# Performance work log

Measured on AMD Instinct MI355X. Metric: run time of the kernel, lower is better.

## Reference

```python
import jax, jax.numpy as jnp
import numpy as np

GROUP = 128  # per-group quantization along the input dimension


def _quantize_int4(w):
    """Asymmetric INT4 per-group quantization. w: [out, in] -> (q, scale, zero).
    q: int32 in [0,15], shape [out, in//GROUP, GROUP]; scale/zero: [out, in//GROUP]."""
    o, i = w.shape
    wg = w.reshape(o, i // GROUP, GROUP)
    mn = wg.min(axis=-1)
    mx = wg.max(axis=-1)
    scale = (mx - mn) / 15.0
    scale = jnp.where(scale == 0, jnp.float32(1.0), scale)
    zero = jnp.clip(jnp.round(-mn / scale), 0.0, 15.0)
    q = jnp.clip(jnp.round(wg / scale[..., None]) + zero[..., None], 0.0, 15.0).astype(jnp.int32)
    return q, scale.astype(jnp.float32), zero.astype(jnp.float32)


def _dequant(q, s, z):
    """(q - zero) * scale, regrouped back to [out, in]."""
    w = (q.astype(jnp.float32) - z[..., None]) * s[..., None]
    return w.reshape(q.shape[0], -1)


def setup_inputs() -> dict:
    key = jax.random.key(0)
    ks = jax.random.split(key, 5)
    B, D_IN, D_H, D_OUT = 512, 2048, 8192, 2048
    x = jax.random.normal(ks[0], (B, D_IN), dtype=jnp.float32)
    w1 = jax.random.normal(ks[1], (D_H, D_IN), dtype=jnp.float32) * 0.02
    b1 = jax.random.normal(ks[2], (D_H,), dtype=jnp.float32) * 0.01
    w2 = jax.random.normal(ks[3], (D_OUT, D_H), dtype=jnp.float32) * 0.02
    b2 = jax.random.normal(ks[4], (D_OUT,), dtype=jnp.float32) * 0.01
    q1, s1, z1 = _quantize_int4(w1)
    q2, s2, z2 = _quantize_int4(w2)
    return {"x": x, "q1": q1, "s1": s1, "z1": z1, "b1": b1,
            "q2": q2, "s2": s2, "z2": z2, "b2": b2}


def reference(x, q1, s1, z1, b1, q2, s2, z2, b2):
    # Layer 1: INT4 dequant + Linear + ReLU (fused in the native kernel)
    w1 = _dequant(q1, s1, z1)              # [D_H, D_IN]
    h = jax.nn.relu(x @ w1.T + b1)         # [B, D_H]
    # Layer 2: INT4 dequant + Linear (no activation)
    w2 = _dequant(q2, s2, z2)              # [D_OUT, D_H]
    return h @ w2.T + b2                   # [B, D_OUT]
```

## Files before the change

### kernel.cpp

```cpp
#include <hip/hip_runtime.h>
#include <stdint.h>

typedef unsigned short u16;
typedef __attribute__((ext_vector_type(8))) short bf16x8;
typedef __attribute__((ext_vector_type(8))) unsigned short u16x8;
typedef __attribute__((ext_vector_type(4))) float f32x4;
typedef __attribute__((ext_vector_type(4))) int i32x4;

__device__ __forceinline__ u16 f2bf(float f) {
  uint32_t u = __builtin_bit_cast(uint32_t, f);
  u += 0x7fffu + ((u >> 16) & 1u);
  return (u16)(u >> 16);
}

#define GLD16(g, l)                                                         \
  __builtin_amdgcn_global_load_lds(                                         \
      (const __attribute__((address_space(1))) void*)(g),                   \
      (__attribute__((address_space(3))) void*)(l), 16, 0, 0)


__global__ __launch_bounds__(256) void cvt_f32_bf16(const float* __restrict__ src,
                                                    u16* __restrict__ dst, int n8) {
  int t = blockIdx.x * 256 + threadIdx.x;
  if (t >= n8) return;
  f32x4 a = ((const f32x4*)src)[2 * t];
  f32x4 b = ((const f32x4*)src)[2 * t + 1];
  u16x8 o;
  o[0] = f2bf(a[0]); o[1] = f2bf(a[1]); o[2] = f2bf(a[2]); o[3] = f2bf(a[3]);
  o[4] = f2bf(b[0]); o[5] = f2bf(b[1]); o[6] = f2bf(b[2]); o[7] = f2bf(b[3]);
  ((u16x8*)dst)[t] = o;
}

__global__ __launch_bounds__(256) void dequant_w(const int* __restrict__ q,
                                                 const float* __restrict__ s,
                                                 const float* __restrict__ z,
                                                 u16* __restrict__ w, int n8) {
  int t = blockIdx.x * 256 + threadIdx.x;
  if (t >= n8) return;
  int g = t >> 4;
  float sc = s[g];
  float zp = z[g];
  i32x4 a = ((const i32x4*)q)[2 * t];
  i32x4 b = ((const i32x4*)q)[2 * t + 1];
  u16x8 o;
  o[0] = f2bf(((float)a[0] - zp) * sc);
  o[1] = f2bf(((float)a[1] - zp) * sc);
  o[2] = f2bf(((float)a[2] - zp) * sc);
  o[3] = f2bf(((float)a[3] - zp) * sc);
  o[4] = f2bf(((float)b[0] - zp) * sc);
  o[5] = f2bf(((float)b[1] - zp) * sc);
  o[6] = f2bf(((float)b[2] - zp) * sc);
  o[7] = f2bf(((float)b[3] - zp) * sc);
  ((u16x8*)w)[t] = o;
}

__global__ __launch_bounds__(256) void bias_init(float* __restrict__ out,
                                                 const float* __restrict__ b,
                                                 int N, int n4) {
  int t = blockIdx.x * 256 + threadIdx.x;
  if (t >= n4) return;
  int idx = t * 4;
  int n = idx & (N - 1);
  *(f32x4*)(out + idx) = *(const f32x4*)(b + n);
}

template <bool RELU, bool OUT_BF16, bool ATOMIC>
__global__ __launch_bounds__(256) void gemm_bt(const u16* __restrict__ A,
                                               const u16* __restrict__ Bm,
                                               const float* __restrict__ bias,
                                               void* __restrict__ Cout,
                                               int M, int N, int K, int kChunk) {
  __shared__ u16 As[128 * 32];
  __shared__ u16 Bs[128 * 32];
  const int tid = threadIdx.x;
  const int wave = tid >> 6;
  const int lane = tid & 63;
  const int m0 = blockIdx.y << 7;
  const int n0 = blockIdx.x << 7;
  const int kStart = blockIdx.z * kChunk;
  const int srow = lane >> 2;
  const int scol = (lane & 3) << 3;
  const int wm = (wave >> 1) << 6;
  const int wn = (wave & 1) << 6;
  const int quad = lane >> 4;
  const int l15 = lane & 15;

  const u16* Ab = A + (size_t)(m0 + 32 * wave + srow) * K + kStart + scol;
  const u16* Bb = Bm + (size_t)(n0 + 32 * wave + srow) * K + kStart + scol;
  u16* AsD0 = &As[(32 * wave + 0) * 32];
  u16* AsD1 = &As[(32 * wave + 16) * 32];
  u16* BsD0 = &Bs[(32 * wave + 0) * 32];
  u16* BsD1 = &Bs[(32 * wave + 16) * 32];
  const size_t rowskip = (size_t)16 * K;

  f32x4 acc[4][4];
#pragma unroll
  for (int i = 0; i < 4; i++)
#pragma unroll
    for (int j = 0; j < 4; j++) acc[i][j] = (f32x4){0.f, 0.f, 0.f, 0.f};

  for (int k = 0; k < kChunk; k += 32) {
    GLD16(Ab + k, AsD0);
    GLD16(Ab + k + rowskip, AsD1);
    GLD16(Bb + k, BsD0);
    GLD16(Bb + k + rowskip, BsD1);
    __syncthreads();
    bf16x8 af[4], bf[4];
#pragma unroll
    for (int i = 0; i < 4; i++)
      af[i] = *(const bf16x8*)&As[(wm + i * 16 + l15) * 32 + quad * 8];
#pragma unroll
    for (int j = 0; j < 4; j++)
      bf[j] = *(const bf16x8*)&Bs[(wn + j * 16 + l15) * 32 + quad * 8];
#pragma unroll
    for (int i = 0; i < 4; i++)
#pragma unroll
      for (int j = 0; j < 4; j++)
        acc[i][j] = __builtin_amdgcn_mfma_f32_16x16x32_bf16(af[i], bf[j], acc[i][j], 0, 0, 0);
    __syncthreads();
  }

#pragma unroll
  for (int i = 0; i < 4; i++) {
#pragma unroll
    for (int j = 0; j < 4; j++) {
      const int col = n0 + wn + j * 16 + l15;
      float bv = 0.f;
      if (!ATOMIC) bv = bias[col];
#pragma unroll
      for (int r = 0; r < 4; r++) {
        const int row = m0 + wm + i * 16 + quad * 4 + r;
        float v = acc[i][j][r];
        if (ATOMIC) {
          atomicAdd((float*)Cout + (size_t)row * N + col, v);
        } else {
          v += bv;
          if (RELU) v = v > 0.f ? v : 0.f;
          if (OUT_BF16)
            ((u16*)Cout)[(size_t)row * N + col] = f2bf(v);
          else
            ((float*)Cout)[(size_t)row * N + col] = v;
        }
      }
    }
  }
}


extern "C" void kernel_launch(void* const* d_in, const int* in_sizes, int n_in,
                              void* d_out, int out_size, void* d_ws, size_t ws_size,
                              hipStream_t stream) {
  const float* x  = (const float*)d_in[0];
  const int*   q1 = (const int*)d_in[1];
  const float* s1 = (const float*)d_in[2];
  const float* z1 = (const float*)d_in[3];
  const float* b1 = (const float*)d_in[4];
  const int*   q2 = (const int*)d_in[5];
  const float* s2 = (const float*)d_in[6];
  const float* z2 = (const float*)d_in[7];
  const float* b2 = (const float*)d_in[8];
  float* out = (float*)d_out;

  const int B = 512, D_IN = 2048, D_H = 8192, D_OUT = 2048;

  char* ws = (char*)d_ws;
  u16* xb  = (u16*)(ws);
  u16* w1b = (u16*)(ws + (size_t)2 * 1024 * 1024);
  u16* hb  = (u16*)(ws + (size_t)34 * 1024 * 1024);
  u16* w2b = (u16*)(ws + (size_t)42 * 1024 * 1024);

  cvt_f32_bf16<<<(B * D_IN / 8 + 255) / 256, 256, 0, stream>>>(x, xb, B * D_IN / 8);
  dequant_w<<<(D_H * D_IN / 8 + 255) / 256, 256, 0, stream>>>(q1, s1, z1, w1b, D_H * D_IN / 8);
  dequant_w<<<(D_OUT * D_H / 8 + 255) / 256, 256, 0, stream>>>(q2, s2, z2, w2b, D_OUT * D_H / 8);
  dim3 g1(D_H / 128, B / 128, 1);
  gemm_bt<true, true, false><<<g1, 256, 0, stream>>>(xb, w1b, b1, hb, B, D_H, D_IN, D_IN);
  bias_init<<<(B * D_OUT / 4 + 255) / 256, 256, 0, stream>>>(out, b2, D_OUT, B * D_OUT / 4);
  dim3 g2(D_OUT / 128, B / 128, 4);
  gemm_bt<false, false, true><<<g2, 256, 0, stream>>>(hb, w2b, nullptr, out, B, D_OUT, D_H, D_H / 4);
}
```

Measured before the change: 276.2 us.

## Triple-buffer LDS in GEMM with swizzled layout and raise split-K

Replaces the single-buffered K loop with a three-stage LDS ring. Global-to-LDS loads for the next tiles are issued ahead and gated with explicit vmcnt waits, so memory latency overlaps with MFMA work. The LDS column index is XOR-swizzled to reduce bank conflicts on fragment reads. The second GEMM's split-K factor goes from 4 to 8 to put more blocks on the device, at the cost of more atomic adds and more LDS per block.

```diff
diff --git a/kernel.cpp b/kernel.cpp
--- a/kernel.cpp
+++ b/kernel.cpp
@@ -70,8 +70,8 @@
                                                const float* __restrict__ bias,
                                                void* __restrict__ Cout,
                                                int M, int N, int K, int kChunk) {
-  __shared__ u16 As[128 * 32];
-  __shared__ u16 Bs[128 * 32];
+  __shared__ u16 As[3][128 * 32];
+  __shared__ u16 Bs[3][128 * 32];
   const int tid = threadIdx.x;
   const int wave = tid >> 6;
   const int lane = tid & 63;
@@ -79,19 +79,18 @@
   const int n0 = blockIdx.x << 7;
   const int kStart = blockIdx.z * kChunk;
   const int srow = lane >> 2;
-  const int scol = (lane & 3) << 3;
+  const int scol = (((lane & 3) ^ ((lane >> 3) & 3)) << 3);
   const int wm = (wave >> 1) << 6;
   const int wn = (wave & 1) << 6;
   const int quad = lane >> 4;
   const int l15 = lane & 15;
+  const int cs = ((quad ^ ((l15 >> 1) & 3)) << 3);
 
   const u16* Ab = A + (size_t)(m0 + 32 * wave + srow) * K + kStart + scol;
   const u16* Bb = Bm + (size_t)(n0 + 32 * wave + srow) * K + kStart + scol;
-  u16* AsD0 = &As[(32 * wave + 0) * 32];
-  u16* AsD1 = &As[(32 * wave + 16) * 32];
-  u16* BsD0 = &Bs[(32 * wave + 0) * 32];
-  u16* BsD1 = &Bs[(32 * wave + 16) * 32];
+  const int ldsW = (32 * wave) * 32;
   const size_t rowskip = (size_t)16 * K;
+  const int nT = kChunk >> 5;
 
   f32x4 acc[4][4];
 #pragma unroll
@@ -99,26 +98,60 @@
 #pragma unroll
     for (int j = 0; j < 4; j++) acc[i][j] = (f32x4){0.f, 0.f, 0.f, 0.f};
 
-  for (int k = 0; k < kChunk; k += 32) {
-    GLD16(Ab + k, AsD0);
-    GLD16(Ab + k + rowskip, AsD1);
-    GLD16(Bb + k, BsD0);
-    GLD16(Bb + k + rowskip, BsD1);
-    __syncthreads();
-    bf16x8 af[4], bf[4];
-#pragma unroll
-    for (int i = 0; i < 4; i++)
-      af[i] = *(const bf16x8*)&As[(wm + i * 16 + l15) * 32 + quad * 8];
-#pragma unroll
-    for (int j = 0; j < 4; j++)
-      bf[j] = *(const bf16x8*)&Bs[(wn + j * 16 + l15) * 32 + quad * 8];
-#pragma unroll
-    for (int i = 0; i < 4; i++)
-#pragma unroll
-      for (int j = 0; j < 4; j++)
-        acc[i][j] = __builtin_amdgcn_mfma_f32_16x16x32_bf16(af[i], bf[j], acc[i][j], 0, 0, 0);
-    __syncthreads();
+#define STAGE(bi_, t_)                                    \
+  do {                                                    \
+    const int ko_ = (t_) << 5;                            \
+    GLD16(Ab + ko_, &As[bi_][ldsW]);                      \
+    GLD16(Ab + ko_ + rowskip, &As[bi_][ldsW + 512]);      \
+    GLD16(Bb + ko_, &Bs[bi_][ldsW]);                      \
+    GLD16(Bb + ko_ + rowskip, &Bs[bi_][ldsW + 512]);      \
+  } while (0)
+
+  bf16x8 af[4], bf[4];
+#define LOADFRAGS(bi_)                                                        \
+  do {                                                                        \
+    _Pragma("unroll") for (int i = 0; i < 4; i++)                             \
+        af[i] = *(const bf16x8*)&As[bi_][(wm + i * 16 + l15) * 32 + cs];      \
+    _Pragma("unroll") for (int j = 0; j < 4; j++)                             \
+        bf[j] = *(const bf16x8*)&Bs[bi_][(wn + j * 16 + l15) * 32 + cs];      \
+  } while (0)
+
+#define DOMFMA()                                                              \
+  do {                                                                        \
+    _Pragma("unroll") for (int i = 0; i < 4; i++)                             \
+        _Pragma("unroll") for (int j = 0; j < 4; j++)                         \
+            acc[i][j] = __builtin_amdgcn_mfma_f32_16x16x32_bf16(              \
+                af[i], bf[j], acc[i][j], 0, 0, 0);                            \
+  } while (0)
+
+  STAGE(0, 0);
+  STAGE(1, 1);
+  STAGE(2, 2);
+
+  int bi = 0;
+  for (int t = 0; t < nT - 2; ++t) {
+    asm volatile("s_waitcnt vmcnt(8)" ::: "memory");
+    __builtin_amdgcn_s_barrier();
+    LOADFRAGS(bi);
+    asm volatile("s_waitcnt lgkmcnt(0)" ::: "memory");
+    __builtin_amdgcn_s_barrier();
+    if (t + 3 < nT) STAGE(bi, t + 3);
+    DOMFMA();
+    bi = (bi == 2) ? 0 : bi + 1;
   }
+  asm volatile("s_waitcnt vmcnt(4)" ::: "memory");
+  __builtin_amdgcn_s_barrier();
+  LOADFRAGS(bi);
+  DOMFMA();
+  bi = (bi == 2) ? 0 : bi + 1;
+  asm volatile("s_waitcnt vmcnt(0)" ::: "memory");
+  __builtin_amdgcn_s_barrier();
+  LOADFRAGS(bi);
+  DOMFMA();
+
+#undef STAGE
+#undef LOADFRAGS
+#undef DOMFMA
 
 #pragma unroll
   for (int i = 0; i < 4; i++) {
@@ -175,6 +208,6 @@
   dim3 g1(D_H / 128, B / 128, 1);
   gemm_bt<true, true, false><<<g1, 256, 0, stream>>>(xb, w1b, b1, hb, B, D_H, D_IN, D_IN);
   bias_init<<<(B * D_OUT / 4 + 255) / 256, 256, 0, stream>>>(out, b2, D_OUT, B * D_OUT / 4);
-  dim3 g2(D_OUT / 128, B / 128, 4);
-  gemm_bt<false, false, true><<<g2, 256, 0, stream>>>(hb, w2b, nullptr, out, B, D_OUT, D_H, D_H / 4);
-}
+  dim3 g2(D_OUT / 128, B / 128, 8);
+  gemm_bt<false, false, true><<<g2, 256, 0, stream>>>(hb, w2b, nullptr, out, B, D_OUT, D_H, D_H / 8);
+}
```

Result: faster. 252.9 us (-8.4%).
